# Optimization experiments

Hardware: AMD Instinct MI355X
Metric: run time of the kernel (lower is better)

Reference implementation:

```python
import jax, jax.numpy as jnp
import numpy as np

B, C, H, W = 8, 256, 64, 64
S = H * W  # dim_spatial = 4096
DQK = 256
DV = 256


def setup_inputs() -> dict:
    key = jax.random.key(0)
    k1, k2, k3, k4, k5 = jax.random.split(key, 5)
    queries = jax.random.normal(k1, (B, DQK, H, W), dtype=jnp.float32)
    keys = jax.random.normal(k2, (B, DQK, H, W), dtype=jnp.float32)
    values = jax.random.normal(k3, (B, DV, H, W), dtype=jnp.float32)
    q_pos = jax.random.normal(k4, (1, S, DQK), dtype=jnp.float32) * 0.05  # 'random_normal' init
    k_pos = jax.random.normal(k5, (1, S, DQK), dtype=jnp.float32) * 0.05
    return {"queries": queries, "keys": keys, "values": values, "q_pos": q_pos, "k_pos": k_pos}


def reference(queries, keys, values, q_pos, k_pos):
    scale = DQK ** (-0.5)
    # NCHW -> (B, S, C)
    q = jnp.transpose(queries, (0, 2, 3, 1)).reshape(-1, S, DQK) + q_pos
    k = jnp.transpose(keys, (0, 2, 3, 1)).reshape(-1, S, DQK) + k_pos
    v = jnp.transpose(values, (0, 2, 3, 1)).reshape(-1, S, DV)
    dots = jnp.einsum('bqd,bkd->bqk', q, k) * scale  # (B, S, S)
    attn = jax.nn.softmax(dots, axis=-1)
    out = jnp.einsum('bqk,bkd->bqd', attn, v)  # (B, S, DV)
    out = jnp.transpose(out, (0, 2, 1)).reshape(values.shape)  # (B, DV, H, W)
    return out
```

## Files before the change

### kernel.cpp

```cpp
#include <hip/hip_runtime.h>
#include <hip/hip_bf16.h>

#define B_N   8
#define S_N   4096
#define D_N   256
#define QBLK  128
#define KVBLK 32
#define NCH   (S_N / KVBLK)
#define IMGSZ 16384
#define SCALE 0.0625f

typedef __attribute__((ext_vector_type(8)))  short bf16x8;
typedef __attribute__((ext_vector_type(16))) float f32x16;

__device__ __forceinline__ void async16(const char* g, char* l) {
  __builtin_amdgcn_global_load_lds(
      (const __attribute__((address_space(1))) void*)g,
      (__attribute__((address_space(3))) void*)l, 16, 0, 0);
}

__device__ __forceinline__ unsigned cvt_pk_bf16(float lo, float hi) {
  unsigned r;
  asm("v_cvt_pk_bf16_f32 %0, %1, %2" : "=v"(r) : "v"(lo), "v"(hi));
  return r;
}
__device__ __forceinline__ void swap32(unsigned& a, unsigned& b) {
  asm("v_permlane32_swap_b32 %0, %1" : "+v"(a), "+v"(b));
}
__device__ __forceinline__ float xhalf_max(float x) {
  float a = x, b = x;
  asm("" : "+v"(b));
  asm("v_permlane32_swap_b32 %0, %1" : "+v"(a), "+v"(b));
  return fmaxf(a, b);
}
__device__ __forceinline__ float xhalf_add(float x) {
  float a = x, b = x;
  asm("" : "+v"(b));
  asm("v_permlane32_swap_b32 %0, %1" : "+v"(a), "+v"(b));
  return a + b;
}

__global__ void prep_qk(const float* __restrict__ src, const float* __restrict__ pos,
                        __hip_bfloat16* __restrict__ dst, float mul) {
  __shared__ float tile[64][65];
  const int b  = blockIdx.z;
  const int s0 = blockIdx.x * 64;
  const int c0 = blockIdx.y * 64;
  const int t  = threadIdx.x;
  const int x  = t & 63;
  const int y4 = t >> 6;
  const float* sp = src + ((size_t)b * D_N + c0) * S_N + s0;
#pragma unroll
  for (int i = 0; i < 16; ++i) {
    int c = y4 + i * 4;
    tile[c][x] = sp[(size_t)c * S_N + x];
  }
  __syncthreads();
  __hip_bfloat16* dp = dst + ((size_t)b * S_N + s0) * D_N + c0;
  const float* pp = pos + (size_t)s0 * D_N + c0;
#pragma unroll
  for (int i = 0; i < 16; ++i) {
    int s = y4 + i * 4;
    float v = (tile[x][s] + pp[(size_t)s * D_N + x]) * mul;
    dp[(size_t)s * D_N + x] = __float2bfloat16(v);
  }
}

__global__ void prep_kimg(const float* __restrict__ src, const float* __restrict__ pos,
                          char* __restrict__ img) {
  __shared__ float tile[64][65];
  const int b  = blockIdx.z;
  const int s0 = blockIdx.x * 64;
  const int c0 = blockIdx.y * 64;
  const int t  = threadIdx.x;
  const int x  = t & 63;
  const int y4 = t >> 6;
  const float* sp = src + ((size_t)b * D_N + c0) * S_N + s0;
#pragma unroll
  for (int i = 0; i < 16; ++i) {
    int c = y4 + i * 4;
    tile[c][x] = sp[(size_t)c * S_N + x];
  }
  __syncthreads();
  const float* pp = pos + (size_t)s0 * D_N + c0;
#pragma unroll
  for (int i = 0; i < 16; ++i) {
    int srow = y4 + i * 4;
    int d    = c0 + x;
    float v  = tile[x][srow] + pp[(size_t)srow * D_N + x];
    int s    = s0 + srow;
    int ch   = s >> 5;
    int row  = s & 31;
    char* dst = img + ((size_t)(b * NCH + ch)) * IMGSZ + row * 512
                + (((d >> 3) ^ (row & 7)) << 4) + (d & 7) * 2;
    *reinterpret_cast<__hip_bfloat16*>(dst) = __float2bfloat16(v);
  }
}

struct alignas(16) bf8s { __hip_bfloat16 v[8]; };
__global__ void prep_vimg(const float* __restrict__ src, char* __restrict__ img) {
  const int ch = blockIdx.x;
  const int b  = blockIdx.y;
  const int t  = threadIdx.x;
  char* ib = img + ((size_t)(b * NCH + ch)) * IMGSZ;
#pragma unroll
  for (int i = 0; i < 4; ++i) {
    int idx = i * 256 + t;
    int d   = idx >> 2;
    int sp  = idx & 3;
    int sl  = sp ^ ((d >> 1) & 3);
    const float* vs = src + ((size_t)b * D_N + d) * S_N + ch * KVBLK + sl * 8;
    float4 a = *reinterpret_cast<const float4*>(vs);
    float4 c = *reinterpret_cast<const float4*>(vs + 4);
    bf8s w;
    w.v[0] = __float2bfloat16(a.x); w.v[1] = __float2bfloat16(a.y);
    w.v[2] = __float2bfloat16(a.z); w.v[3] = __float2bfloat16(a.w);
    w.v[4] = __float2bfloat16(c.x); w.v[5] = __float2bfloat16(c.y);
    w.v[6] = __float2bfloat16(c.z); w.v[7] = __float2bfloat16(c.w);
    *reinterpret_cast<bf8s*>(ib + d * 64 + sp * 16) = w;
  }
}

#define LDS_BYTES 32768

__global__ __launch_bounds__(256, 2) void attn_kernel(
    const __hip_bfloat16* __restrict__ Qb, const char* __restrict__ Kt,
    const char* __restrict__ Vt, float* __restrict__ P0,
    float2* __restrict__ mlbuf, float* __restrict__ out) {
  __shared__ __align__(16) char lds[LDS_BYTES];

  const int tid  = threadIdx.x;
  const int wave = tid >> 6;
  const int lane = tid & 63;
  const int l31  = lane & 31;
  const int h    = lane >> 5;

  const int lin = blockIdx.x;
  const int b   = lin & 7;
  const int kvh = (lin >> 3) & 1;
  const int qt  = lin >> 4;
  const int q0  = qt * QBLK + wave * 32;

  bf16x8 qf[16];
  {
    const __hip_bfloat16* qp = Qb + ((size_t)b * S_N + q0 + l31) * D_N + h * 8;
#pragma unroll
    for (int kc = 0; kc < 16; ++kc)
      qf[kc] = *reinterpret_cast<const bf16x8*>(qp + kc * 16);
  }

  f32x16 o[8];
#pragma unroll
  for (int df = 0; df < 8; ++df)
#pragma unroll
    for (int r = 0; r < 16; ++r) o[df][r] = 0.f;
  float m_ = -1e30f, l_ = 0.f;

  const char* kimgB = Kt + (size_t)b * NCH * IMGSZ;
  const char* vimgB = Vt + (size_t)b * NCH * IMGSZ;

  for (int t = kvh * (NCH / 2); t < (kvh + 1) * (NCH / 2); ++t) {
    __syncthreads();
    if (wave < 2) {
      const char* s = kimgB + (size_t)t * IMGSZ;
#pragma unroll
      for (int i = 0; i < 8; ++i) {
        int c = wave * 8 + i;
        async16(s + c * 1024 + lane * 16, lds + c * 1024);
      }
    } else {
      const char* s = vimgB + (size_t)t * IMGSZ;
#pragma unroll
      for (int i = 0; i < 8; ++i) {
        int c = (wave - 2) * 8 + i;
        async16(s + c * 1024 + lane * 16, lds + 16384 + c * 1024);
      }
    }
    __syncthreads();

    const char* Klds = lds;
    const char* Vlds = lds + 16384;

    f32x16 se;
#pragma unroll
    for (int r = 0; r < 16; ++r) se[r] = 0.f;
    {
      const char* kr = Klds + l31 * 512;
      const int swz = (l31 & 7) << 4;
#pragma unroll
      for (int kc = 0; kc < 16; ++kc) {
        bf16x8 kf = *reinterpret_cast<const bf16x8*>(kr + ((kc * 32 + h * 16) ^ swz));
        se = __builtin_amdgcn_mfma_f32_32x32x16_bf16(kf, qf[kc], se, 0, 0, 0);
      }
    }

    float t8[8];
#pragma unroll
    for (int i = 0; i < 8; ++i) t8[i] = fmaxf(se[i], se[i + 8]);
    float pm = fmaxf(fmaxf(fmaxf(t8[0], t8[1]), fmaxf(t8[2], t8[3])),
                     fmaxf(fmaxf(t8[4], t8[5]), fmaxf(t8[6], t8[7])));
    float pmax = xhalf_max(pm);

    if (!__all(pmax <= m_ + 8.f)) {
      float mn = fmaxf(m_, pmax);
      float al = __expf(m_ - mn);
      m_ = mn;
      l_ *= al;
#pragma unroll
      for (int df = 0; df < 8; ++df)
#pragma unroll
        for (int r = 0; r < 16; ++r) o[df][r] *= al;
    }
#pragma unroll
    for (int r = 0; r < 16; ++r) se[r] = __expf(se[r] - m_);
    float s8[8];
#pragma unroll
    for (int i = 0; i < 8; ++i) s8[i] = se[i] + se[i + 8];
    float rs = ((s8[0] + s8[1]) + (s8[2] + s8[3])) + ((s8[4] + s8[5]) + (s8[6] + s8[7]));
    l_ += xhalf_add(rs);

    union U8 { unsigned u[4]; bf16x8 v; };
    U8 pb[2];
    {
      unsigned u0 = cvt_pk_bf16(se[0],  se[1]);
      unsigned v0 = cvt_pk_bf16(se[4],  se[5]);
      swap32(u0, v0);
      unsigned u1 = cvt_pk_bf16(se[2],  se[3]);
      unsigned v1 = cvt_pk_bf16(se[6],  se[7]);
      swap32(u1, v1);
      pb[0].u[0] = u0; pb[0].u[1] = u1; pb[0].u[2] = v0; pb[0].u[3] = v1;
      unsigned u2 = cvt_pk_bf16(se[8],  se[9]);
      unsigned v2 = cvt_pk_bf16(se[12], se[13]);
      swap32(u2, v2);
      unsigned u3 = cvt_pk_bf16(se[10], se[11]);
      unsigned v3 = cvt_pk_bf16(se[14], se[15]);
      swap32(u3, v3);
      pb[1].u[0] = u2; pb[1].u[1] = u3; pb[1].u[2] = v2; pb[1].u[3] = v3;
    }

#pragma unroll
    for (int df = 0; df < 8; ++df) {
      const int d = df * 32 + l31;
      const char* vr = Vlds + d * 64;
      const int dx = (d >> 1) & 3;
#pragma unroll
      for (int kf = 0; kf < 2; ++kf) {
        bf16x8 vf = *reinterpret_cast<const bf16x8*>(vr + (((kf * 2 + h) ^ dx) << 4));
        o[df] = __builtin_amdgcn_mfma_f32_32x32x16_bf16(vf, pb[kf].v, o[df], 0, 0, 0);
      }
    }
  }

  if (h == 0)
    mlbuf[(size_t)(kvh * B_N + b) * S_N + q0 + l31] = make_float2(m_, l_);
  float* pdst = (kvh ? out : P0) + (size_t)b * D_N * S_N + q0 + l31;
#pragma unroll
  for (int df = 0; df < 8; ++df)
#pragma unroll
    for (int r = 0; r < 16; ++r) {
      int d = df * 32 + (r & 3) + 8 * (r >> 2) + 4 * h;
      pdst[(size_t)d * S_N] = o[df][r];
    }
}

__global__ void merge_w(const float2* __restrict__ mlbuf, float2* __restrict__ wbuf) {
  int i = blockIdx.x * 256 + threadIdx.x;
  float2 a = mlbuf[i];
  float2 c = mlbuf[(size_t)B_N * S_N + i];
  float ms = fmaxf(a.x, c.x);
  float c0 = __expf(a.x - ms), c1 = __expf(c.x - ms);
  float inv = 1.0f / (c0 * a.y + c1 * c.y);
  wbuf[i] = make_float2(c0 * inv, c1 * inv);
}

__global__ void merge_o(const float* __restrict__ P0, const float2* __restrict__ wbuf,
                        float* __restrict__ out) {
  int i = blockIdx.x * 256 + threadIdx.x;
  float4 p0 = reinterpret_cast<const float4*>(P0)[i];
  float4 p1 = reinterpret_cast<float4*>(out)[i];
  int b  = i >> 18;
  int s4 = i & (S_N / 4 - 1);
  const float2* wb = wbuf + (size_t)b * S_N + s4 * 4;
  float2 w0 = wb[0], w1 = wb[1], w2 = wb[2], w3 = wb[3];
  float4 r;
  r.x = w0.x * p0.x + w0.y * p1.x;
  r.y = w1.x * p0.y + w1.y * p1.y;
  r.z = w2.x * p0.z + w2.y * p1.z;
  r.w = w3.x * p0.w + w3.y * p1.w;
  reinterpret_cast<float4*>(out)[i] = r;
}

extern "C" void kernel_launch(void* const* d_in, const int* in_sizes, int n_in,
                              void* d_out, int out_size, void* d_ws, size_t ws_size,
                              hipStream_t stream) {
  const float* queries = (const float*)d_in[0];
  const float* keys    = (const float*)d_in[1];
  const float* values  = (const float*)d_in[2];
  const float* q_pos   = (const float*)d_in[3];
  const float* k_pos   = (const float*)d_in[4];
  float* out = (float*)d_out;

  const size_t per = (size_t)B_N * S_N * D_N;
  __hip_bfloat16* Qb = (__hip_bfloat16*)d_ws;
  char*   Kt    = (char*)d_ws + per * 2;
  char*   Vt    = Kt + per * 2;
  float*  P0    = (float*)(Vt + per * 2);
  float2* mlbuf = (float2*)((char*)P0 + per * 4);
  float2* wbuf  = mlbuf + (size_t)2 * B_N * S_N;

  prep_qk  <<<dim3(S_N / 64, D_N / 64, B_N), 256, 0, stream>>>(queries, q_pos, Qb, SCALE);
  prep_kimg<<<dim3(S_N / 64, D_N / 64, B_N), 256, 0, stream>>>(keys,    k_pos, Kt);
  prep_vimg<<<dim3(NCH, B_N), 256, 0, stream>>>(values, Vt);
  attn_kernel<<<dim3((S_N / QBLK) * B_N * 2), 256, 0, stream>>>(Qb, Kt, Vt, P0, mlbuf, out);
  merge_w<<<dim3(B_N * S_N / 256), 256, 0, stream>>>(mlbuf, wbuf);
  merge_o<<<dim3((unsigned)(per / 4 / 256)), 256, 0, stream>>>(P0, wbuf, out);
}
```

Measured before the change: 202.0 us.

## Double-buffer K/V LDS tiles to overlap async loads with MFMA compute

The K/V staging buffer in LDS grows to two halves. The loop now issues the async global->LDS load for the next chunk before computing on the current one, waiting with s_waitcnt vmcnt(8) so only the current chunk's loads must have landed. This hides global load latency behind the QK and PV MFMAs. It doubles LDS use to 64KB per block, which may limit occupancy under launch_bounds(256,2), and it relies on manual waitcnt and barrier placement being correct.

```diff
diff --git a/kernel.cpp b/kernel.cpp
--- a/kernel.cpp
+++ b/kernel.cpp
@@ -121,7 +121,7 @@
   }
 }
 
-#define LDS_BYTES 32768
+#define LDS_BYTES 65536
 
 __global__ __launch_bounds__(256, 2) void attn_kernel(
     const __hip_bfloat16* __restrict__ Qb, const char* __restrict__ Kt,
@@ -140,6 +140,7 @@
   const int kvh = (lin >> 3) & 1;
   const int qt  = lin >> 4;
   const int q0  = qt * QBLK + wave * 32;
+  const int t0  = kvh * (NCH / 2);
 
   bf16x8 qf[16];
   {
@@ -159,27 +160,40 @@
   const char* kimgB = Kt + (size_t)b * NCH * IMGSZ;
   const char* vimgB = Vt + (size_t)b * NCH * IMGSZ;
 
-  for (int t = kvh * (NCH / 2); t < (kvh + 1) * (NCH / 2); ++t) {
-    __syncthreads();
+  auto STAGE = [&](int buf, int tt) {
+    char* base = lds + buf * 32768;
     if (wave < 2) {
-      const char* s = kimgB + (size_t)t * IMGSZ;
+      const char* s = kimgB + (size_t)(t0 + tt) * IMGSZ;
 #pragma unroll
       for (int i = 0; i < 8; ++i) {
         int c = wave * 8 + i;
-        async16(s + c * 1024 + lane * 16, lds + c * 1024);
+        async16(s + c * 1024 + lane * 16, base + c * 1024);
       }
     } else {
-      const char* s = vimgB + (size_t)t * IMGSZ;
+      const char* s = vimgB + (size_t)(t0 + tt) * IMGSZ;
 #pragma unroll
       for (int i = 0; i < 8; ++i) {
         int c = (wave - 2) * 8 + i;
-        async16(s + c * 1024 + lane * 16, lds + 16384 + c * 1024);
+        async16(s + c * 1024 + lane * 16, base + 16384 + c * 1024);
       }
     }
-    __syncthreads();
-
-    const char* Klds = lds;
-    const char* Vlds = lds + 16384;
+  };
+
+  STAGE(0, 0);
+
+  for (int t = 0; t < NCH / 2; ++t) {
+    const int cur = t & 1;
+    if (t + 1 < NCH / 2) {
+      STAGE(cur ^ 1, t + 1);
+      asm volatile("s_waitcnt vmcnt(8)" ::: "memory");
+    } else {
+      asm volatile("s_waitcnt vmcnt(0)" ::: "memory");
+    }
+    __builtin_amdgcn_s_barrier();
+    __builtin_amdgcn_sched_barrier(0);
+
+    const char* Klds = lds + cur * 32768;
+    const char* Vlds = Klds + 16384;
 
     f32x16 se;
 #pragma unroll
@@ -249,6 +263,8 @@
         o[df] = __builtin_amdgcn_mfma_f32_32x32x16_bf16(vf, pb[kf].v, o[df], 0, 0, 0);
       }
     }
+
+    __builtin_amdgcn_s_barrier();
   }
 
   if (h == 0)
```

After: 307.5 us. +52.2%, slower.
